# Performance work log

Hardware: AMD Instinct MI355X
Metric: run time of the kernel (lower is better)

The kernel has to match this reference:

```python
import jax, jax.numpy as jnp
import numpy as np

D_MODEL = 1024
N_HEAD = 16
D_HEAD = 64
D_CAT = N_HEAD * D_HEAD
HD_MLP = 4096
LN_EPS = 1e-5


def setup_inputs() -> dict:
    key = jax.random.key(0)
    ks = jax.random.split(key, 12)
    bn, t = 2, 2048
    s = lambda fan_in: 1.0 / np.sqrt(fan_in)
    return {
        "x": jax.random.normal(ks[0], (bn, t, D_MODEL), dtype=jnp.float32),
        "mask": jnp.ones((bn, t), dtype=jnp.int32),
        "w_qkv": jax.random.normal(ks[1], (D_MODEL, 3 * D_CAT), dtype=jnp.float32) * s(D_MODEL),
        "w_tail": jax.random.normal(ks[2], (D_CAT, D_MODEL), dtype=jnp.float32) * s(D_CAT),
        "b_tail": jnp.zeros((D_MODEL,), dtype=jnp.float32),
        "ln1_g": jnp.ones((D_MODEL,), dtype=jnp.float32),
        "ln1_b": jnp.zeros((D_MODEL,), dtype=jnp.float32),
        "ln2_g": jnp.ones((D_MODEL,), dtype=jnp.float32),
        "ln2_b": jnp.zeros((D_MODEL,), dtype=jnp.float32),
        "w1": jax.random.normal(ks[3], (D_MODEL, HD_MLP), dtype=jnp.float32) * s(D_MODEL),
        "b1": jnp.zeros((HD_MLP,), dtype=jnp.float32),
        "w2": jax.random.normal(ks[4], (HD_MLP, D_MODEL), dtype=jnp.float32) * s(HD_MLP),
        "b2": jnp.zeros((D_MODEL,), dtype=jnp.float32),
    }


def _layer_norm(x, g, b):
    mu = jnp.mean(x, axis=-1, keepdims=True)
    var = jnp.mean(jnp.square(x - mu), axis=-1, keepdims=True)
    return (x - mu) * jax.lax.rsqrt(var + LN_EPS) * g + b


def _attention(z, mask, w_qkv, w_tail, b_tail):
    bn, t, _ = z.shape
    qkv = z @ w_qkv                      # (bn, t, 3*d_cat)
    qkv = qkv.reshape(bn, t, N_HEAD, 3, D_HEAD)  # chunk layout: per-head [q|k|v]
    q = qkv[..., 0, :].transpose(0, 2, 1, 3)     # (bn, h, t, dh)
    k = qkv[..., 1, :].transpose(0, 2, 1, 3)
    v = qkv[..., 2, :].transpose(0, 2, 1, 3)
    scale = D_HEAD ** -0.5
    dots = jnp.einsum("bhqd,bhkd->bhqk", q, k) * scale
    key_mask = (mask == 0)[:, None, None, :]     # (bn,1,1,t)
    dots = jnp.where(key_mask, -jnp.inf, dots)
    coef = jax.nn.softmax(dots, axis=-1)
    attn = jnp.einsum("bhqk,bhkd->bhqd", coef, v)
    out = attn.transpose(0, 2, 1, 3).reshape(bn, t, D_CAT)
    return out @ w_tail + b_tail


def reference(x, mask, w_qkv, w_tail, b_tail, ln1_g, ln1_b, ln2_g, ln2_b, w1, b1, w2, b2):
    z = _layer_norm(x, ln1_g, ln1_b)
    x = _attention(z, mask, w_qkv, w_tail, b_tail) + x
    z = _layer_norm(x, ln2_g, ln2_b)
    h = jax.nn.gelu(z @ w1 + b1, approximate=False)  # torch GELU default = exact erf
    x = h @ w2 + b2 + x
    return x
```

## Files before the change

kernel.cpp:

```cpp
#include <hip/hip_runtime.h>
#include <hip/hip_bf16.h>

#define DM 1024
#define TT 2048
#define NH 16
#define DH 64
#define HD 4096

typedef __attribute__((ext_vector_type(4))) float f32x4;
typedef __attribute__((ext_vector_type(8))) short s16x8;
typedef __attribute__((ext_vector_type(4))) short s16x4;

static __device__ __forceinline__ short f2bf(float f) {
  __hip_bfloat16 h = __float2bfloat16(f);
  return *reinterpret_cast<short*>(&h);
}

typedef const __attribute__((address_space(1))) char* gas1_t;
typedef __attribute__((address_space(3))) char* las3_t;
static __device__ __forceinline__ void glds16(const void* g, void* l) {
  __builtin_amdgcn_global_load_lds((gas1_t)g, (las3_t)l, 16, 0, 0);
}

__global__ __launch_bounds__(256) void transpose_cvt_k(
    const float* __restrict__ in, short* __restrict__ out, int K, int N)
{
  __shared__ float tile[32][33];
  const int n0 = blockIdx.x * 32, k0 = blockIdx.y * 32;
  const int tx = threadIdx.x & 31, ty = threadIdx.x >> 5;
#pragma unroll
  for (int i = 0; i < 4; ++i)
    tile[ty + i * 8][tx] = in[(size_t)(k0 + ty + i * 8) * N + n0 + tx];
  __syncthreads();
#pragma unroll
  for (int i = 0; i < 4; ++i) {
    int n = ty + i * 8;
    out[(size_t)(n0 + n) * K + k0 + tx] = f2bf(tile[tx][n]);
  }
}

__global__ __launch_bounds__(256) void ln_k(
    const float* __restrict__ x, const float* __restrict__ g,
    const float* __restrict__ b, short* __restrict__ out)
{
  const int row = blockIdx.x;
  const int tid = threadIdx.x;
  const float4 v = ((const float4*)(x + (size_t)row * DM))[tid];
  float s = v.x + v.y + v.z + v.w;
  float q = v.x * v.x + v.y * v.y + v.z * v.z + v.w * v.w;
#pragma unroll
  for (int off = 1; off < 64; off <<= 1) {
    s += __shfl_xor(s, off);
    q += __shfl_xor(q, off);
  }
  __shared__ float ss[4], sq[4];
  const int wave = tid >> 6;
  if ((tid & 63) == 0) { ss[wave] = s; sq[wave] = q; }
  __syncthreads();
  s = ss[0] + ss[1] + ss[2] + ss[3];
  q = sq[0] + sq[1] + sq[2] + sq[3];
  const float mu = s * (1.0f / DM);
  const float var = q * (1.0f / DM) - mu * mu;
  const float rs = rsqrtf(var + 1e-5f);
  const float4 gv = ((const float4*)g)[tid];
  const float4 bv = ((const float4*)b)[tid];
  s16x4 o;
  o[0] = f2bf((v.x - mu) * rs * gv.x + bv.x);
  o[1] = f2bf((v.y - mu) * rs * gv.y + bv.y);
  o[2] = f2bf((v.z - mu) * rs * gv.z + bv.z);
  o[3] = f2bf((v.w - mu) * rs * gv.w + bv.w);
  *(s16x4*)(out + (size_t)row * DM + tid * 4) = o;
}

template<int EPI, int BN>
__global__ __launch_bounds__(256) void gemm_bt(
    const short* __restrict__ A, const short* __restrict__ B,
    const float* __restrict__ bias, const float* __restrict__ res,
    float* __restrict__ outF, short* __restrict__ outB,
    short* __restrict__ outK, short* __restrict__ outV,
    int M, int N, int K)
{
  constexpr int MR = (BN == 128) ? 4 : 2;
  __shared__ short As[2][128 * 32];
  __shared__ short Bs[2][BN * 32];
  const int tid = threadIdx.x;
  const int wave = tid >> 6, lane = tid & 63;
  const int l15 = lane & 15, lhi = lane >> 4;
  const int bm = blockIdx.x, bn = blockIdx.y;
  const int wr = (BN == 128) ? (wave >> 1) : wave;
  const int wc = (BN == 128) ? (wave & 1) : 0;
  f32x4 acc[MR][4] = {};

  const int sr = wave * 16 + (lane >> 2);
  const int schunk = ((lane & 3) ^ ((lane >> 3) & 3)) * 16;
  const char* gA = (const char*)(A + (size_t)(bm * 128 + sr) * K) + schunk;
  const char* gB = (const char*)(B + (size_t)(bn * BN + sr) * K) + schunk;
  const size_t rowstep = (size_t)64 * K * 2;

  const int NK = K >> 5;
  const int rsw = (l15 >> 1) & 3;
  const int achunk = (lhi ^ rsw) << 4;

  auto stage = [&](int buf, int kt) {
    const size_t koff = (size_t)kt * 64;
    char* lA = (char*)As[buf] + wave * 1024;
    glds16(gA + koff, lA);
    glds16(gA + koff + rowstep, lA + 4096);
    char* lB = (char*)Bs[buf] + wave * 1024;
    glds16(gB + koff, lB);
    if (BN == 128) glds16(gB + koff + rowstep, lB + 4096);
  };

  stage(0, 0);
  __syncthreads();
  int cur = 0;
  for (int kt = 0; kt < NK; ++kt) {
    if (kt + 1 < NK) stage(cur ^ 1, kt + 1);
    s16x8 af[MR], bfv[4];
#pragma unroll
    for (int m = 0; m < MR; ++m) {
      const int row = wr * (MR * 16) + m * 16 + l15;
      af[m] = *(const s16x8*)((const char*)As[cur] + row * 64 + achunk);
    }
#pragma unroll
    for (int n = 0; n < 4; ++n) {
      const int row = wc * 64 + n * 16 + l15;
      bfv[n] = *(const s16x8*)((const char*)Bs[cur] + row * 64 + achunk);
    }
#pragma unroll
    for (int m = 0; m < MR; ++m)
#pragma unroll
      for (int n = 0; n < 4; ++n)
        acc[m][n] = __builtin_amdgcn_mfma_f32_16x16x32_bf16(af[m], bfv[n], acc[m][n], 0, 0, 0);
    __syncthreads();
    cur ^= 1;
  }

  const int rowb = bm * 128 + wr * (MR * 16);
  const int colb = bn * BN + wc * 64;
#pragma unroll
  for (int m = 0; m < MR; ++m) {
#pragma unroll
    for (int n = 0; n < 4; ++n) {
      if (EPI == 3) {
        const int col0 = colb + n * 16;
        const int h = col0 / 192;
        const int c0 = col0 - h * 192;
        const int region = c0 >> 6;
        const int d = (c0 & 63) + l15;
        const int row0 = rowb + m * 16 + lhi * 4;
        const int bb = row0 >> 11, tl0 = row0 & 2047;
        const size_t bh = (size_t)bb * NH + h;
        if (region == 2) {
          s16x4 pk;
#pragma unroll
          for (int rr = 0; rr < 4; ++rr) pk[rr] = f2bf(acc[m][n][rr]);
          *(s16x4*)(outV + (bh * 64 + d) * TT + tl0) = pk;
        } else {
          short* dst = (region == 0) ? outB : outK;
          const float qs = (region == 0) ? 0.18033688011112042f : 1.0f;
#pragma unroll
          for (int rr = 0; rr < 4; ++rr)
            dst[(bh * TT + tl0 + rr) * 64 + d] = f2bf(acc[m][n][rr] * qs);
        }
      } else {
        const int col = colb + n * 16 + l15;
        const float bv = bias[col];
#pragma unroll
        for (int rr = 0; rr < 4; ++rr) {
          const int row = rowb + m * 16 + lhi * 4 + rr;
          float v = acc[m][n][rr] + bv;
          if (EPI == 1) v += res[(size_t)row * N + col];
          if (EPI == 2) v = 0.5f * v * (1.0f + erff(v * 0.70710678118f));
          if (EPI == 1) outF[(size_t)row * N + col] = v;
          else outB[(size_t)row * N + col] = f2bf(v);
        }
      }
    }
  }
}

__global__ __launch_bounds__(256) void attn_k(
    const short* __restrict__ Qb, const short* __restrict__ Kb,
    const short* __restrict__ Vtb, const int* __restrict__ mask,
    short* __restrict__ outp)
{
  const int tid = threadIdx.x, wave = tid >> 6, lane = tid & 63;
  const int l15 = lane & 15, lhi = lane >> 4;
  const int lb = blockIdx.x;
  const int r = lb & 31;
  const int bh = (r & 7) * 4 + (r >> 3);
  const int b = bh >> 4, h = bh & 15;
  const int q0 = (lb >> 5) * 64;

  __shared__ short Ks[128 * 64];
  __shared__ short Vt[64 * 128];
  __shared__ short Ps[4][16 * 128];

  const short* qbase = Qb + ((size_t)bh * TT + q0 + wave * 16 + l15) * 64;
  const s16x8 aq0 = *(const s16x8*)(qbase + lhi * 8);
  const s16x8 aq1 = *(const s16x8*)(qbase + 32 + lhi * 8);

  f32x4 o[4] = {};
  float mrow = -1e30f, lrow = 0.f;

  const int kr_s = tid >> 1, kc_s = (tid & 1) * 32;
  const int ksw = (kr_s & 7) << 4;
  const int vr_s = tid >> 2, vc_s = (tid & 3) * 32;
  const int vsw = (vr_s & 7) << 4;

  const short* kgb = Kb + (size_t)bh * TT * 64 + (size_t)kr_s * 64 + kc_s;
  const short* vgb = Vtb + ((size_t)bh * 64 + vr_s) * TT + vc_s;

  s16x8 kpre[4], vpre[4];
#pragma unroll
  for (int j = 0; j < 4; ++j) {
    kpre[j] = *(const s16x8*)(kgb + j * 8);
    vpre[j] = *(const s16x8*)(vgb + j * 8);
  }
  int m0 = mask[b * TT + lane], m1 = mask[b * TT + 64 + lane];

  for (int t0 = 0; t0 < TT; t0 += 128) {
    char* krow = (char*)Ks + kr_s * 128;
#pragma unroll
    for (int j = 0; j < 4; ++j)
      *(s16x8*)(krow + ((kc_s * 2 + j * 16) ^ ksw)) = kpre[j];
    char* vrow = (char*)Vt + vr_s * 256;
#pragma unroll
    for (int j = 0; j < 4; ++j)
      *(s16x8*)(vrow + ((vc_s * 2 + j * 16) ^ vsw)) = vpre[j];
    __syncthreads();

    const unsigned long long mb0 = __ballot(m0 != 0);
    const unsigned long long mb1 = __ballot(m1 != 0);
    const bool full = (mb0 & mb1) == ~0ULL;

    if (t0 + 128 < TT) {
      const short* kg = kgb + (size_t)(t0 + 128) * 64;
      const short* vg = vgb + t0 + 128;
#pragma unroll
      for (int j = 0; j < 4; ++j) {
        kpre[j] = *(const s16x8*)(kg + j * 8);
        vpre[j] = *(const s16x8*)(vg + j * 8);
      }
      m0 = mask[b * TT + t0 + 128 + lane];
      m1 = mask[b * TT + t0 + 192 + lane];
    }

    f32x4 sv[8];
#pragma unroll
    for (int n = 0; n < 8; ++n) {
      const int row = n * 16 + l15;
      const int sw = (row & 7) << 4;
      const char* kr = (const char*)Ks + row * 128;
      const s16x8 a0 = *(const s16x8*)(kr + ((lhi * 16) ^ sw));
      const s16x8 a1 = *(const s16x8*)(kr + ((64 + lhi * 16) ^ sw));
      f32x4 z = {};
      z = __builtin_amdgcn_mfma_f32_16x16x32_bf16(a0, aq0, z, 0, 0, 0);
      z = __builtin_amdgcn_mfma_f32_16x16x32_bf16(a1, aq1, z, 0, 0, 0);
      sv[n] = z;
    }

    if (!full) {
#pragma unroll
      for (int n = 0; n < 8; ++n) {
        const unsigned long long mbn = (n < 4) ? mb0 : mb1;
        const unsigned nib = (unsigned)(mbn >> ((n & 3) * 16 + lhi * 4)) & 0xF;
#pragma unroll
        for (int rr = 0; rr < 4; ++rr)
          if (!((nib >> rr) & 1)) sv[n][rr] = -3e38f;
      }
    }
    float mx0 = -3e38f, mx1 = -3e38f, mx2 = -3e38f, mx3 = -3e38f;
#pragma unroll
    for (int n = 0; n < 8; ++n) {
      mx0 = fmaxf(mx0, sv[n][0]); mx1 = fmaxf(mx1, sv[n][1]);
      mx2 = fmaxf(mx2, sv[n][2]); mx3 = fmaxf(mx3, sv[n][3]);
    }
    float mx = fmaxf(fmaxf(mx0, mx1), fmaxf(mx2, mx3));
    mx = fmaxf(mx, __shfl_xor(mx, 16));
    mx = fmaxf(mx, __shfl_xor(mx, 32));

    if (__any(mx > mrow + 8.0f)) {
      const float mn = fmaxf(mrow, mx);
      const float alpha = exp2f(mrow - mn);
      mrow = mn;
      lrow *= alpha;
      float ar[4];
#pragma unroll
      for (int rr = 0; rr < 4; ++rr) ar[rr] = __shfl(alpha, lhi * 4 + rr);
#pragma unroll
      for (int db = 0; db < 4; ++db)
#pragma unroll
        for (int rr = 0; rr < 4; ++rr) o[db][rr] *= ar[rr];
    }

    float s0 = 0.f, s1 = 0.f, s2 = 0.f, s3 = 0.f;
#pragma unroll
    for (int n = 0; n < 8; ++n) {
      sv[n][0] = exp2f(sv[n][0] - mrow); s0 += sv[n][0];
      sv[n][1] = exp2f(sv[n][1] - mrow); s1 += sv[n][1];
      sv[n][2] = exp2f(sv[n][2] - mrow); s2 += sv[n][2];
      sv[n][3] = exp2f(sv[n][3] - mrow); s3 += sv[n][3];
    }
    float sum = (s0 + s1) + (s2 + s3);
    sum += __shfl_xor(sum, 16);
    sum += __shfl_xor(sum, 32);
    lrow += sum;

    char* pbase = (char*)Ps + wave * 4096 + l15 * 256;
    const int swp = (l15 & 7) << 4;
#pragma unroll
    for (int n = 0; n < 8; ++n) {
      s16x4 pk;
#pragma unroll
      for (int rr = 0; rr < 4; ++rr) pk[rr] = f2bf(sv[n][rr]);
      *(s16x4*)(pbase + ((n * 32 + lhi * 8) ^ swp)) = pk;
    }
    asm volatile("s_waitcnt lgkmcnt(0)" ::: "memory");
    __builtin_amdgcn_sched_barrier(0);
    s16x8 ap[4];
#pragma unroll
    for (int ks = 0; ks < 4; ++ks)
      ap[ks] = *(const s16x8*)(pbase + ((ks * 64 + lhi * 16) ^ swp));
#pragma unroll
    for (int db = 0; db < 4; ++db) {
      const int d = db * 16 + l15;
      const int swv = (d & 7) << 4;
      const char* vr2 = (const char*)Vt + d * 256;
#pragma unroll
      for (int ks = 0; ks < 4; ++ks) {
        const s16x8 bv = *(const s16x8*)(vr2 + ((ks * 64 + lhi * 16) ^ swv));
        o[db] = __builtin_amdgcn_mfma_f32_16x16x32_bf16(ap[ks], bv, o[db], 0, 0, 0);
      }
    }
    __syncthreads();
  }

  float lr[4];
#pragma unroll
  for (int rr = 0; rr < 4; ++rr) lr[rr] = __shfl(lrow, lhi * 4 + rr);
#pragma unroll
  for (int db = 0; db < 4; ++db) {
#pragma unroll
    for (int rr = 0; rr < 4; ++rr) {
      const int qg = q0 + wave * 16 + lhi * 4 + rr;
      const int cg = h * 64 + db * 16 + l15;
      outp[(size_t)(b * TT + qg) * DM + cg] = f2bf(o[db][rr] / lr[rr]);
    }
  }
}

extern "C" void kernel_launch(void* const* d_in, const int* in_sizes, int n_in,
                              void* d_out, int out_size, void* d_ws, size_t ws_size,
                              hipStream_t stream)
{
  const float* x      = (const float*)d_in[0];
  const int*   mask   = (const int*)d_in[1];
  const float* w_qkv  = (const float*)d_in[2];
  const float* w_tail = (const float*)d_in[3];
  const float* b_tail = (const float*)d_in[4];
  const float* ln1g   = (const float*)d_in[5];
  const float* ln1b   = (const float*)d_in[6];
  const float* ln2g   = (const float*)d_in[7];
  const float* ln2b   = (const float*)d_in[8];
  const float* w1     = (const float*)d_in[9];
  const float* b1     = (const float*)d_in[10];
  const float* w2     = (const float*)d_in[11];
  const float* b2     = (const float*)d_in[12];

  char* ws = (char*)d_ws;
  size_t off = 0;
  auto take = [&](size_t bytes) {
    char* p = ws + off;
    off += (bytes + 255) & ~(size_t)255;
    return p;
  };
  short* slotW = (short*)take((size_t)4096 * 2048 * 2);
  short* slotZ = (short*)take((size_t)4096 * 1024 * 2);
  short* qb    = (short*)take((size_t)32 * 2048 * 64 * 2);
  short* kb    = (short*)take((size_t)32 * 2048 * 64 * 2);
  short* vtb   = (short*)take((size_t)32 * 64 * 2048 * 2);
  float* x1    = (float*)take((size_t)4096 * 1024 * 4);
  short* hbuf  = (short*)take((size_t)4096 * 4096 * 2);

  transpose_cvt_k<<<dim3(3072 / 32, 1024 / 32), 256, 0, stream>>>(w_qkv, slotW, 1024, 3072);
  ln_k<<<4096, 256, 0, stream>>>(x, ln1g, ln1b, slotZ);
  gemm_bt<3, 128><<<dim3(32, 24), 256, 0, stream>>>(slotZ, slotW, nullptr, nullptr,
                                                    nullptr, qb, kb, vtb, 4096, 3072, 1024);
  attn_k<<<1024, 256, 0, stream>>>(qb, kb, vtb, mask, slotZ);
  transpose_cvt_k<<<dim3(1024 / 32, 1024 / 32), 256, 0, stream>>>(w_tail, slotW, 1024, 1024);
  gemm_bt<1, 64><<<dim3(32, 16), 256, 0, stream>>>(slotZ, slotW, b_tail, x,
                                                   x1, nullptr, nullptr, nullptr, 4096, 1024, 1024);
  ln_k<<<4096, 256, 0, stream>>>(x1, ln2g, ln2b, slotZ);
  transpose_cvt_k<<<dim3(4096 / 32, 1024 / 32), 256, 0, stream>>>(w1, slotW, 1024, 4096);
  gemm_bt<2, 128><<<dim3(32, 32), 256, 0, stream>>>(slotZ, slotW, b1, nullptr,
                                                    nullptr, hbuf, nullptr, nullptr, 4096, 4096, 1024);
  transpose_cvt_k<<<dim3(1024 / 32, 4096 / 32), 256, 0, stream>>>(w2, slotW, 4096, 1024);
  gemm_bt<1, 64><<<dim3(32, 16), 256, 0, stream>>>(hbuf, slotW, b2, x1,
                                                   (float*)d_out, nullptr, nullptr, nullptr, 4096, 1024, 4096);
}
```

Baseline: 294.3 us.

## Restructure attention: two query tiles per wave, K/V read directly from global

The attention kernel no longer stages K and V in shared memory behind block barriers. Each wave now loads K and V fragments straight from global memory (relying on cache) and processes two 16-row query tiles, so every K/V fragment feeds twice as many MFMAs. V fragments for the next head-dim block are prefetched in software, and the grid is halved to 512 blocks with a launch-bounds occupancy hint. This removes the LDS staging and __syncthreads cost, but trades it for more global/L2 traffic, since the four waves of a block each fetch K/V themselves, plus higher register pressure.

```diff
diff --git a/kernel.cpp b/kernel.cpp
--- a/kernel.cpp
+++ b/kernel.cpp
@@ -180,7 +180,7 @@
   }
 }
 
-__global__ __launch_bounds__(256) void attn_k(
+__global__ __launch_bounds__(256, 2) void attn_k(
     const short* __restrict__ Qb, const short* __restrict__ Kb,
     const short* __restrict__ Vtb, const int* __restrict__ mask,
     short* __restrict__ outp)
@@ -188,77 +188,48 @@
   const int tid = threadIdx.x, wave = tid >> 6, lane = tid & 63;
   const int l15 = lane & 15, lhi = lane >> 4;
   const int lb = blockIdx.x;
-  const int r = lb & 31;
-  const int bh = (r & 7) * 4 + (r >> 3);
+  const int bh = lb & 31, qb = lb >> 5;
   const int b = bh >> 4, h = bh & 15;
-  const int q0 = (lb >> 5) * 64;
-
-  __shared__ short Ks[128 * 64];
-  __shared__ short Vt[64 * 128];
-  __shared__ short Ps[4][16 * 128];
-
-  const short* qbase = Qb + ((size_t)bh * TT + q0 + wave * 16 + l15) * 64;
-  const s16x8 aq0 = *(const s16x8*)(qbase + lhi * 8);
-  const s16x8 aq1 = *(const s16x8*)(qbase + 32 + lhi * 8);
-
-  f32x4 o[4] = {};
-  float mrow = -1e30f, lrow = 0.f;
-
-  const int kr_s = tid >> 1, kc_s = (tid & 1) * 32;
-  const int ksw = (kr_s & 7) << 4;
-  const int vr_s = tid >> 2, vc_s = (tid & 3) * 32;
-  const int vsw = (vr_s & 7) << 4;
-
-  const short* kgb = Kb + (size_t)bh * TT * 64 + (size_t)kr_s * 64 + kc_s;
-  const short* vgb = Vtb + ((size_t)bh * 64 + vr_s) * TT + vc_s;
-
-  s16x8 kpre[4], vpre[4];
-#pragma unroll
-  for (int j = 0; j < 4; ++j) {
-    kpre[j] = *(const s16x8*)(kgb + j * 8);
-    vpre[j] = *(const s16x8*)(vgb + j * 8);
-  }
-  int m0 = mask[b * TT + lane], m1 = mask[b * TT + 64 + lane];
+  const int qw = qb * 128 + wave * 32;
+
+  __shared__ short Ps[4][2][16 * 128];
+
+  const short* qb0 = Qb + ((size_t)bh * TT + qw + l15) * 64;
+  const short* qb1 = qb0 + 16 * 64;
+  const s16x8 aq00 = *(const s16x8*)(qb0 + lhi * 8);
+  const s16x8 aq01 = *(const s16x8*)(qb0 + 32 + lhi * 8);
+  const s16x8 aq10 = *(const s16x8*)(qb1 + lhi * 8);
+  const s16x8 aq11 = *(const s16x8*)(qb1 + 32 + lhi * 8);
+
+  f32x4 o[2][4] = {};
+  float mrow[2] = {-1e30f, -1e30f};
+  float lrow[2] = {0.f, 0.f};
+
+  const short* kgb = Kb + (size_t)bh * TT * 64;
+  const short* vgb = Vtb + (size_t)bh * 64 * TT;
+  const int swp = (l15 & 7) << 4;
+  char* pb0 = (char*)Ps + wave * 8192 + l15 * 256;
+  char* pb1 = pb0 + 4096;
 
   for (int t0 = 0; t0 < TT; t0 += 128) {
-    char* krow = (char*)Ks + kr_s * 128;
-#pragma unroll
-    for (int j = 0; j < 4; ++j)
-      *(s16x8*)(krow + ((kc_s * 2 + j * 16) ^ ksw)) = kpre[j];
-    char* vrow = (char*)Vt + vr_s * 256;
-#pragma unroll
-    for (int j = 0; j < 4; ++j)
-      *(s16x8*)(vrow + ((vc_s * 2 + j * 16) ^ vsw)) = vpre[j];
-    __syncthreads();
-
+    const int m0 = mask[b * TT + t0 + lane];
+    const int m1 = mask[b * TT + t0 + 64 + lane];
     const unsigned long long mb0 = __ballot(m0 != 0);
     const unsigned long long mb1 = __ballot(m1 != 0);
     const bool full = (mb0 & mb1) == ~0ULL;
 
-    if (t0 + 128 < TT) {
-      const short* kg = kgb + (size_t)(t0 + 128) * 64;
-      const short* vg = vgb + t0 + 128;
-#pragma unroll
-      for (int j = 0; j < 4; ++j) {
-        kpre[j] = *(const s16x8*)(kg + j * 8);
-        vpre[j] = *(const s16x8*)(vg + j * 8);
-      }
-      m0 = mask[b * TT + t0 + 128 + lane];
-      m1 = mask[b * TT + t0 + 192 + lane];
-    }
-
-    f32x4 sv[8];
+    f32x4 sv0[8], sv1[8];
 #pragma unroll
     for (int n = 0; n < 8; ++n) {
-      const int row = n * 16 + l15;
-      const int sw = (row & 7) << 4;
-      const char* kr = (const char*)Ks + row * 128;
-      const s16x8 a0 = *(const s16x8*)(kr + ((lhi * 16) ^ sw));
-      const s16x8 a1 = *(const s16x8*)(kr + ((64 + lhi * 16) ^ sw));
-      f32x4 z = {};
-      z = __builtin_amdgcn_mfma_f32_16x16x32_bf16(a0, aq0, z, 0, 0, 0);
-      z = __builtin_amdgcn_mfma_f32_16x16x32_bf16(a1, aq1, z, 0, 0, 0);
-      sv[n] = z;
+      const short* kr = kgb + (size_t)(t0 + n * 16 + l15) * 64 + lhi * 8;
+      const s16x8 ka0 = *(const s16x8*)kr;
+      const s16x8 ka1 = *(const s16x8*)(kr + 32);
+      f32x4 z0 = {}, z1 = {};
+      z0 = __builtin_amdgcn_mfma_f32_16x16x32_bf16(ka0, aq00, z0, 0, 0, 0);
+      z0 = __builtin_amdgcn_mfma_f32_16x16x32_bf16(ka1, aq01, z0, 0, 0, 0);
+      z1 = __builtin_amdgcn_mfma_f32_16x16x32_bf16(ka0, aq10, z1, 0, 0, 0);
+      z1 = __builtin_amdgcn_mfma_f32_16x16x32_bf16(ka1, aq11, z1, 0, 0, 0);
+      sv0[n] = z0; sv1[n] = z1;
     }
 
     if (!full) {
@@ -268,85 +239,101 @@
         const unsigned nib = (unsigned)(mbn >> ((n & 3) * 16 + lhi * 4)) & 0xF;
 #pragma unroll
         for (int rr = 0; rr < 4; ++rr)
-          if (!((nib >> rr) & 1)) sv[n][rr] = -3e38f;
-      }
-    }
-    float mx0 = -3e38f, mx1 = -3e38f, mx2 = -3e38f, mx3 = -3e38f;
+          if (!((nib >> rr) & 1)) { sv0[n][rr] = -3e38f; sv1[n][rr] = -3e38f; }
+      }
+    }
+
+#pragma unroll
+    for (int f = 0; f < 2; ++f) {
+      f32x4* sv = f ? sv1 : sv0;
+      float mx0 = -3e38f, mx1 = -3e38f, mx2 = -3e38f, mx3 = -3e38f;
+#pragma unroll
+      for (int n = 0; n < 8; ++n) {
+        mx0 = fmaxf(mx0, sv[n][0]); mx1 = fmaxf(mx1, sv[n][1]);
+        mx2 = fmaxf(mx2, sv[n][2]); mx3 = fmaxf(mx3, sv[n][3]);
+      }
+      float mx = fmaxf(fmaxf(mx0, mx1), fmaxf(mx2, mx3));
+      mx = fmaxf(mx, __shfl_xor(mx, 16));
+      mx = fmaxf(mx, __shfl_xor(mx, 32));
+      if (__any(mx > mrow[f] + 8.0f)) {
+        const float mn = fmaxf(mrow[f], mx);
+        const float alpha = exp2f(mrow[f] - mn);
+        mrow[f] = mn;
+        lrow[f] *= alpha;
+        float ar[4];
+#pragma unroll
+        for (int rr = 0; rr < 4; ++rr) ar[rr] = __shfl(alpha, lhi * 4 + rr);
+#pragma unroll
+        for (int db = 0; db < 4; ++db)
+#pragma unroll
+          for (int rr = 0; rr < 4; ++rr) o[f][db][rr] *= ar[rr];
+      }
+      float s0 = 0.f, s1 = 0.f, s2 = 0.f, s3 = 0.f;
+#pragma unroll
+      for (int n = 0; n < 8; ++n) {
+        sv[n][0] = exp2f(sv[n][0] - mrow[f]); s0 += sv[n][0];
+        sv[n][1] = exp2f(sv[n][1] - mrow[f]); s1 += sv[n][1];
+        sv[n][2] = exp2f(sv[n][2] - mrow[f]); s2 += sv[n][2];
+        sv[n][3] = exp2f(sv[n][3] - mrow[f]); s3 += sv[n][3];
+      }
+      float sum = (s0 + s1) + (s2 + s3);
+      sum += __shfl_xor(sum, 16);
+      sum += __shfl_xor(sum, 32);
+      lrow[f] += sum;
+    }
+
 #pragma unroll
     for (int n = 0; n < 8; ++n) {
-      mx0 = fmaxf(mx0, sv[n][0]); mx1 = fmaxf(mx1, sv[n][1]);
-      mx2 = fmaxf(mx2, sv[n][2]); mx3 = fmaxf(mx3, sv[n][3]);
-    }
-    float mx = fmaxf(fmaxf(mx0, mx1), fmaxf(mx2, mx3));
-    mx = fmaxf(mx, __shfl_xor(mx, 16));
-    mx = fmaxf(mx, __shfl_xor(mx, 32));
-
-    if (__any(mx > mrow + 8.0f)) {
-      const float mn = fmaxf(mrow, mx);
-      const float alpha = exp2f(mrow - mn);
-      mrow = mn;
-      lrow *= alpha;
-      float ar[4];
-#pragma unroll
-      for (int rr = 0; rr < 4; ++rr) ar[rr] = __shfl(alpha, lhi * 4 + rr);
-#pragma unroll
-      for (int db = 0; db < 4; ++db)
-#pragma unroll
-        for (int rr = 0; rr < 4; ++rr) o[db][rr] *= ar[rr];
-    }
-
-    float s0 = 0.f, s1 = 0.f, s2 = 0.f, s3 = 0.f;
-#pragma unroll
-    for (int n = 0; n < 8; ++n) {
-      sv[n][0] = exp2f(sv[n][0] - mrow); s0 += sv[n][0];
-      sv[n][1] = exp2f(sv[n][1] - mrow); s1 += sv[n][1];
-      sv[n][2] = exp2f(sv[n][2] - mrow); s2 += sv[n][2];
-      sv[n][3] = exp2f(sv[n][3] - mrow); s3 += sv[n][3];
-    }
-    float sum = (s0 + s1) + (s2 + s3);
-    sum += __shfl_xor(sum, 16);
-    sum += __shfl_xor(sum, 32);
-    lrow += sum;
-
-    char* pbase = (char*)Ps + wave * 4096 + l15 * 256;
-    const int swp = (l15 & 7) << 4;
-#pragma unroll
-    for (int n = 0; n < 8; ++n) {
-      s16x4 pk;
-#pragma unroll
-      for (int rr = 0; rr < 4; ++rr) pk[rr] = f2bf(sv[n][rr]);
-      *(s16x4*)(pbase + ((n * 32 + lhi * 8) ^ swp)) = pk;
-    }
+      s16x4 p0, p1;
+#pragma unroll
+      for (int rr = 0; rr < 4; ++rr) { p0[rr] = f2bf(sv0[n][rr]); p1[rr] = f2bf(sv1[n][rr]); }
+      *(s16x4*)(pb0 + ((n * 32 + lhi * 8) ^ swp)) = p0;
+      *(s16x4*)(pb1 + ((n * 32 + lhi * 8) ^ swp)) = p1;
+    }
+    const short* vr0 = vgb + (size_t)l15 * TT + t0 + lhi * 8;
+    s16x8 bvc[4], bvn[4];
+#pragma unroll
+    for (int ks = 0; ks < 4; ++ks) bvc[ks] = *(const s16x8*)(vr0 + ks * 32);
+
     asm volatile("s_waitcnt lgkmcnt(0)" ::: "memory");
     __builtin_amdgcn_sched_barrier(0);
-    s16x8 ap[4];
-#pragma unroll
-    for (int ks = 0; ks < 4; ++ks)
-      ap[ks] = *(const s16x8*)(pbase + ((ks * 64 + lhi * 16) ^ swp));
+    s16x8 ap0[4], ap1[4];
+#pragma unroll
+    for (int ks = 0; ks < 4; ++ks) {
+      ap0[ks] = *(const s16x8*)(pb0 + ((ks * 64 + lhi * 16) ^ swp));
+      ap1[ks] = *(const s16x8*)(pb1 + ((ks * 64 + lhi * 16) ^ swp));
+    }
+
 #pragma unroll
     for (int db = 0; db < 4; ++db) {
-      const int d = db * 16 + l15;
-      const int swv = (d & 7) << 4;
-      const char* vr2 = (const char*)Vt + d * 256;
+      if (db < 3) {
+        const short* vrn = vgb + (size_t)(db * 16 + 16 + l15) * TT + t0 + lhi * 8;
+#pragma unroll
+        for (int ks = 0; ks < 4; ++ks) bvn[ks] = *(const s16x8*)(vrn + ks * 32);
+      }
 #pragma unroll
       for (int ks = 0; ks < 4; ++ks) {
-        const s16x8 bv = *(const s16x8*)(vr2 + ((ks * 64 + lhi * 16) ^ swv));
-        o[db] = __builtin_amdgcn_mfma_f32_16x16x32_bf16(ap[ks], bv, o[db], 0, 0, 0);
-      }
-    }
-    __syncthreads();
-  }
-
-  float lr[4];
-#pragma unroll
-  for (int rr = 0; rr < 4; ++rr) lr[rr] = __shfl(lrow, lhi * 4 + rr);
-#pragma unroll
-  for (int db = 0; db < 4; ++db) {
-#pragma unroll
-    for (int rr = 0; rr < 4; ++rr) {
-      const int qg = q0 + wave * 16 + lhi * 4 + rr;
-      const int cg = h * 64 + db * 16 + l15;
-      outp[(size_t)(b * TT + qg) * DM + cg] = f2bf(o[db][rr] / lr[rr]);
+        o[0][db] = __builtin_amdgcn_mfma_f32_16x16x32_bf16(ap0[ks], bvc[ks], o[0][db], 0, 0, 0);
+        o[1][db] = __builtin_amdgcn_mfma_f32_16x16x32_bf16(ap1[ks], bvc[ks], o[1][db], 0, 0, 0);
+      }
+#pragma unroll
+      for (int ks = 0; ks < 4; ++ks) bvc[ks] = bvn[ks];
+    }
+  }
+
+#pragma unroll
+  for (int f = 0; f < 2; ++f) {
+    float lr[4];
+#pragma unroll
+    for (int rr = 0; rr < 4; ++rr) lr[rr] = __shfl(lrow[f], lhi * 4 + rr);
+#pragma unroll
+    for (int db = 0; db < 4; ++db) {
+#pragma unroll
+      for (int rr = 0; rr < 4; ++rr) {
+        const int qg = qw + f * 16 + lhi * 4 + rr;
+        const int cg = h * 64 + db * 16 + l15;
+        outp[(size_t)(b * TT + qg) * DM + cg] = f2bf(o[f][db][rr] / lr[rr]);
+      }
     }
   }
 }
@@ -388,7 +375,7 @@
   ln_k<<<4096, 256, 0, stream>>>(x, ln1g, ln1b, slotZ);
   gemm_bt<3, 128><<<dim3(32, 24), 256, 0, stream>>>(slotZ, slotW, nullptr, nullptr,
                                                     nullptr, qb, kb, vtb, 4096, 3072, 1024);
-  attn_k<<<1024, 256, 0, stream>>>(qb, kb, vtb, mask, slotZ);
+  attn_k<<<512, 256, 0, stream>>>(qb, kb, vtb, mask, slotZ);
   transpose_cvt_k<<<dim3(1024 / 32, 1024 / 32), 256, 0, stream>>>(w_tail, slotW, 1024, 1024);
   gemm_bt<1, 64><<<dim3(32, 16), 256, 0, stream>>>(slotZ, slotW, b_tail, x,
                                                    x1, nullptr, nullptr, nullptr, 4096, 1024, 1024);
```

Measured after the change: 340.2 us. +15.6%, slower.

## Halve attention KV tile to 64 keys, raise occupancy, pad P buffer, add setprio

Applied to the files above, without the earlier changes.

The attention kernel now streams K/V in 64-key tiles instead of 128. This halves shared memory and the prefetch registers, and launch bounds now request 4 blocks per SM. The P staging buffer uses a padded stride in place of the XOR swizzle, MFMA sections are wrapped in s_setprio, and the block-to-head mapping is simplified. In exchange there are twice as many loop iterations and barriers, and the new mapping may change L2 locality for K/V.

```diff
diff --git a/kernel.cpp b/kernel.cpp
--- a/kernel.cpp
+++ b/kernel.cpp
@@ -180,7 +180,9 @@
   }
 }
 
-__global__ __launch_bounds__(256) void attn_k(
+#define PSTRIDE 144
+#define PFRAG   2304
+__global__ __launch_bounds__(256, 4) void attn_k(
     const short* __restrict__ Qb, const short* __restrict__ Kb,
     const short* __restrict__ Vtb, const int* __restrict__ mask,
     short* __restrict__ outp)
@@ -188,68 +190,58 @@
   const int tid = threadIdx.x, wave = tid >> 6, lane = tid & 63;
   const int l15 = lane & 15, lhi = lane >> 4;
   const int lb = blockIdx.x;
-  const int r = lb & 31;
-  const int bh = (r & 7) * 4 + (r >> 3);
+  const int bh = lb & 31, qb = lb >> 5;
   const int b = bh >> 4, h = bh & 15;
-  const int q0 = (lb >> 5) * 64;
-
-  __shared__ short Ks[128 * 64];
-  __shared__ short Vt[64 * 128];
-  __shared__ short Ps[4][16 * 128];
-
-  const short* qbase = Qb + ((size_t)bh * TT + q0 + wave * 16 + l15) * 64;
-  const s16x8 aq0 = *(const s16x8*)(qbase + lhi * 8);
-  const s16x8 aq1 = *(const s16x8*)(qbase + 32 + lhi * 8);
+  const int qw = qb * 64 + wave * 16;
+
+  __shared__ short Ks[64 * 64];
+  __shared__ short Vt[64 * 64];
+  __shared__ char Ps[4 * PFRAG];
+
+  const short* qp = Qb + ((size_t)bh * TT + qw + l15) * 64;
+  const s16x8 aq0 = *(const s16x8*)(qp + lhi * 8);
+  const s16x8 aq1 = *(const s16x8*)(qp + 32 + lhi * 8);
 
   f32x4 o[4] = {};
   float mrow = -1e30f, lrow = 0.f;
 
-  const int kr_s = tid >> 1, kc_s = (tid & 1) * 32;
+  const int kr_s = tid >> 2, kc_s = (tid & 3) * 16;
   const int ksw = (kr_s & 7) << 4;
-  const int vr_s = tid >> 2, vc_s = (tid & 3) * 32;
-  const int vsw = (vr_s & 7) << 4;
 
   const short* kgb = Kb + (size_t)bh * TT * 64 + (size_t)kr_s * 64 + kc_s;
-  const short* vgb = Vtb + ((size_t)bh * 64 + vr_s) * TT + vc_s;
-
-  s16x8 kpre[4], vpre[4];
-#pragma unroll
-  for (int j = 0; j < 4; ++j) {
-    kpre[j] = *(const s16x8*)(kgb + j * 8);
-    vpre[j] = *(const s16x8*)(vgb + j * 8);
-  }
-  int m0 = mask[b * TT + lane], m1 = mask[b * TT + 64 + lane];
-
-  for (int t0 = 0; t0 < TT; t0 += 128) {
+  const short* vgb = Vtb + ((size_t)bh * 64 + kr_s) * TT + kc_s;
+
+  s16x8 kpre[2], vpre[2];
+  kpre[0] = *(const s16x8*)kgb;       kpre[1] = *(const s16x8*)(kgb + 8);
+  vpre[0] = *(const s16x8*)vgb;       vpre[1] = *(const s16x8*)(vgb + 8);
+  int m0 = mask[b * TT + lane];
+
+  char* pb = Ps + wave * PFRAG + l15 * PSTRIDE;
+
+  for (int t0 = 0; t0 < TT; t0 += 64) {
     char* krow = (char*)Ks + kr_s * 128;
-#pragma unroll
-    for (int j = 0; j < 4; ++j)
-      *(s16x8*)(krow + ((kc_s * 2 + j * 16) ^ ksw)) = kpre[j];
-    char* vrow = (char*)Vt + vr_s * 256;
-#pragma unroll
-    for (int j = 0; j < 4; ++j)
-      *(s16x8*)(vrow + ((vc_s * 2 + j * 16) ^ vsw)) = vpre[j];
+    *(s16x8*)(krow + ((kc_s * 2) ^ ksw)) = kpre[0];
+    *(s16x8*)(krow + ((kc_s * 2 + 16) ^ ksw)) = kpre[1];
+    char* vrow = (char*)Vt + kr_s * 128;
+    *(s16x8*)(vrow + ((kc_s * 2) ^ ksw)) = vpre[0];
+    *(s16x8*)(vrow + ((kc_s * 2 + 16) ^ ksw)) = vpre[1];
     __syncthreads();
 
     const unsigned long long mb0 = __ballot(m0 != 0);
-    const unsigned long long mb1 = __ballot(m1 != 0);
-    const bool full = (mb0 & mb1) == ~0ULL;
-
-    if (t0 + 128 < TT) {
-      const short* kg = kgb + (size_t)(t0 + 128) * 64;
-      const short* vg = vgb + t0 + 128;
-#pragma unroll
-      for (int j = 0; j < 4; ++j) {
-        kpre[j] = *(const s16x8*)(kg + j * 8);
-        vpre[j] = *(const s16x8*)(vg + j * 8);
-      }
-      m0 = mask[b * TT + t0 + 128 + lane];
-      m1 = mask[b * TT + t0 + 192 + lane];
-    }
-
-    f32x4 sv[8];
-#pragma unroll
-    for (int n = 0; n < 8; ++n) {
+    const bool full = mb0 == ~0ULL;
+
+    if (t0 + 64 < TT) {
+      const short* kg = kgb + (size_t)(t0 + 64) * 64;
+      const short* vg = vgb + t0 + 64;
+      kpre[0] = *(const s16x8*)kg;  kpre[1] = *(const s16x8*)(kg + 8);
+      vpre[0] = *(const s16x8*)vg;  vpre[1] = *(const s16x8*)(vg + 8);
+      m0 = mask[b * TT + t0 + 64 + lane];
+    }
+
+    f32x4 sv[4];
+    __builtin_amdgcn_s_setprio(1);
+#pragma unroll
+    for (int n = 0; n < 4; ++n) {
       const int row = n * 16 + l15;
       const int sw = (row & 7) << 4;
       const char* kr = (const char*)Ks + row * 128;
@@ -260,27 +252,27 @@
       z = __builtin_amdgcn_mfma_f32_16x16x32_bf16(a1, aq1, z, 0, 0, 0);
       sv[n] = z;
     }
+    __builtin_amdgcn_s_setprio(0);
 
     if (!full) {
 #pragma unroll
-      for (int n = 0; n < 8; ++n) {
-        const unsigned long long mbn = (n < 4) ? mb0 : mb1;
-        const unsigned nib = (unsigned)(mbn >> ((n & 3) * 16 + lhi * 4)) & 0xF;
+      for (int n = 0; n < 4; ++n) {
+        const unsigned nib = (unsigned)(mb0 >> (n * 16 + lhi * 4)) & 0xF;
 #pragma unroll
         for (int rr = 0; rr < 4; ++rr)
           if (!((nib >> rr) & 1)) sv[n][rr] = -3e38f;
       }
     }
-    float mx0 = -3e38f, mx1 = -3e38f, mx2 = -3e38f, mx3 = -3e38f;
-#pragma unroll
-    for (int n = 0; n < 8; ++n) {
-      mx0 = fmaxf(mx0, sv[n][0]); mx1 = fmaxf(mx1, sv[n][1]);
-      mx2 = fmaxf(mx2, sv[n][2]); mx3 = fmaxf(mx3, sv[n][3]);
-    }
+
+    float mx0 = fmaxf(sv[0][0], sv[1][0]), mx1 = fmaxf(sv[0][1], sv[1][1]);
+    float mx2 = fmaxf(sv[0][2], sv[1][2]), mx3 = fmaxf(sv[0][3], sv[1][3]);
+    mx0 = fmaxf(mx0, fmaxf(sv[2][0], sv[3][0]));
+    mx1 = fmaxf(mx1, fmaxf(sv[2][1], sv[3][1]));
+    mx2 = fmaxf(mx2, fmaxf(sv[2][2], sv[3][2]));
+    mx3 = fmaxf(mx3, fmaxf(sv[2][3], sv[3][3]));
     float mx = fmaxf(fmaxf(mx0, mx1), fmaxf(mx2, mx3));
     mx = fmaxf(mx, __shfl_xor(mx, 16));
     mx = fmaxf(mx, __shfl_xor(mx, 32));
-
     if (__any(mx > mrow + 8.0f)) {
       const float mn = fmaxf(mrow, mx);
       const float alpha = exp2f(mrow - mn);
@@ -294,10 +286,9 @@
 #pragma unroll
         for (int rr = 0; rr < 4; ++rr) o[db][rr] *= ar[rr];
     }
-
     float s0 = 0.f, s1 = 0.f, s2 = 0.f, s3 = 0.f;
 #pragma unroll
-    for (int n = 0; n < 8; ++n) {
+    for (int n = 0; n < 4; ++n) {
       sv[n][0] = exp2f(sv[n][0] - mrow); s0 += sv[n][0];
       sv[n][1] = exp2f(sv[n][1] - mrow); s1 += sv[n][1];
       sv[n][2] = exp2f(sv[n][2] - mrow); s2 += sv[n][2];
@@ -308,32 +299,32 @@
     sum += __shfl_xor(sum, 32);
     lrow += sum;
 
-    char* pbase = (char*)Ps + wave * 4096 + l15 * 256;
-    const int swp = (l15 & 7) << 4;
-#pragma unroll
-    for (int n = 0; n < 8; ++n) {
+#pragma unroll
+    for (int n = 0; n < 4; ++n) {
       s16x4 pk;
 #pragma unroll
       for (int rr = 0; rr < 4; ++rr) pk[rr] = f2bf(sv[n][rr]);
-      *(s16x4*)(pbase + ((n * 32 + lhi * 8) ^ swp)) = pk;
+      *(s16x4*)(pb + n * 32 + lhi * 8) = pk;
     }
     asm volatile("s_waitcnt lgkmcnt(0)" ::: "memory");
     __builtin_amdgcn_sched_barrier(0);
-    s16x8 ap[4];
-#pragma unroll
-    for (int ks = 0; ks < 4; ++ks)
-      ap[ks] = *(const s16x8*)(pbase + ((ks * 64 + lhi * 16) ^ swp));
+    s16x8 ap[2];
+    ap[0] = *(const s16x8*)(pb + lhi * 16);
+    ap[1] = *(const s16x8*)(pb + 64 + lhi * 16);
+
+    __builtin_amdgcn_s_setprio(1);
 #pragma unroll
     for (int db = 0; db < 4; ++db) {
       const int d = db * 16 + l15;
       const int swv = (d & 7) << 4;
-      const char* vr2 = (const char*)Vt + d * 256;
-#pragma unroll
-      for (int ks = 0; ks < 4; ++ks) {
+      const char* vr2 = (const char*)Vt + d * 128;
+#pragma unroll
+      for (int ks = 0; ks < 2; ++ks) {
         const s16x8 bv = *(const s16x8*)(vr2 + ((ks * 64 + lhi * 16) ^ swv));
         o[db] = __builtin_amdgcn_mfma_f32_16x16x32_bf16(ap[ks], bv, o[db], 0, 0, 0);
       }
     }
+    __builtin_amdgcn_s_setprio(0);
     __syncthreads();
   }
 
@@ -344,7 +335,7 @@
   for (int db = 0; db < 4; ++db) {
 #pragma unroll
     for (int rr = 0; rr < 4; ++rr) {
-      const int qg = q0 + wave * 16 + lhi * 4 + rr;
+      const int qg = qw + lhi * 4 + rr;
       const int cg = h * 64 + db * 16 + l15;
       outp[(size_t)(b * TT + qg) * DM + cg] = f2bf(o[db][rr] / lr[rr]);
     }
```

Measured after the change: 285.8 us. -2.9%, faster.
